# Performance work log

Hardware: AMD Instinct MI355X
Metric: run time of the kernel (lower is better)

## Reference

```python
import jax, jax.numpy as jnp
import numpy as np

B, N, C = 8, 2048, 256
E = 32768
H, C_OUT = 8, 64
NEG_SLOPE = 0.2


def setup_inputs() -> dict:
    key = jax.random.key(0)
    k1, k2, k3, k4, k5 = jax.random.split(key, 5)
    x = jax.random.normal(k1, (B, N, C), dtype=jnp.float32)
    edge_index = jax.random.randint(k2, (2, E), 0, N, dtype=jnp.int64)
    W_lin = jax.random.normal(k3, (C, H * C_OUT), dtype=jnp.float32) * 0.05
    att_src = jax.random.normal(k4, (H, C_OUT), dtype=jnp.float32) * 0.05
    att_dst = jax.random.normal(k5, (H, C_OUT), dtype=jnp.float32) * 0.05
    bias = jnp.zeros((H * C_OUT,), dtype=jnp.float32)
    return {"x": x, "edge_index": edge_index, "W_lin": W_lin,
            "att_src": att_src, "att_dst": att_dst, "bias": bias}


def _segment_softmax(logits, segment_ids, num_segments):
    # stable softmax over edges grouped by destination node
    seg_max = jax.ops.segment_max(logits, segment_ids, num_segments=num_segments)
    logits = logits - seg_max[segment_ids]
    exp = jnp.exp(logits)
    seg_sum = jax.ops.segment_sum(exp, segment_ids, num_segments=num_segments)
    return exp / (seg_sum[segment_ids] + 1e-16)


def reference(x, edge_index, W_lin, att_src, att_dst, bias):
    Bn = B * N
    # node linear projection -> [B*N, H, C_out]
    xt = (x.reshape(Bn, C) @ W_lin).reshape(Bn, H, C_OUT)

    # batch the shared edge_index: block b offset by b*N, then append self-loops
    offs = (jnp.arange(B, dtype=edge_index.dtype) * N)[None, :, None]  # [1,B,1]
    ei = (edge_index[:, None, :] + offs).reshape(2, B * E)              # [2,B*E]
    loops = jnp.arange(Bn, dtype=edge_index.dtype)
    src = jnp.concatenate([ei[0], loops])
    dst = jnp.concatenate([ei[1], loops])

    x_j = xt[src]  # [E_tot, H, C_out] source features
    x_i = xt[dst]
    alpha = jnp.einsum('ehc,hc->eh', x_j, att_src) + jnp.einsum('ehc,hc->eh', x_i, att_dst)
    alpha = jax.nn.leaky_relu(alpha, NEG_SLOPE)
    alpha = _segment_softmax(alpha, dst, Bn)  # softmax over incoming edges per node/head

    msg = x_j * alpha[:, :, None]
    out = jax.ops.segment_sum(msg, dst, num_segments=Bn)  # [B*N, H, C_out]
    out = out.reshape(B, N, H * C_OUT) + bias
    return out
```

## Files before the change

kernel.cpp:

```cpp
#include <hip/hip_runtime.h>
#include <hip/hip_bf16.h>

#define BDIM 8
#define NNODE 2048
#define CIN 256
#define NEDGE 32768
#define NHEAD 8
#define COUT 64
#define HC 512
#define BN_TOT 16384
#define NEG_SLOPE 0.2f
#define GEMM_BLKS 256
#define SCAT_BLKS 64
#define CAP 64

typedef __hip_bfloat16 bf16;
typedef __attribute__((ext_vector_type(8))) short bfrag;
typedef __attribute__((ext_vector_type(4))) float ffrag;
typedef float f32x2 __attribute__((ext_vector_type(2)));
typedef float fv4 __attribute__((ext_vector_type(4)));

static __device__ __forceinline__ short f2b(float f) {
    __hip_bfloat16 h = __float2bfloat16(f);
    return *(short*)&h;
}
static __device__ __forceinline__ unsigned pack2(float a, float b) {
    return (unsigned)(unsigned short)f2b(a) | ((unsigned)(unsigned short)f2b(b) << 16);
}
static __device__ __forceinline__ void pkfma(f32x2& a, f32x2 x, f32x2 w) {
    asm("v_pk_fma_f32 %0, %1, %2, %0" : "+v"(a) : "v"(x), "v"(w));
}
static __device__ __forceinline__ f32x2 unpack2(unsigned v) {
    f32x2 r;
    r.x = __uint_as_float(v << 16);
    r.y = __uint_as_float(v & 0xffff0000u);
    return r;
}
static __device__ __forceinline__ void async_cp16(const short* gsrc, short* ldst) {
    __builtin_amdgcn_global_load_lds(
        (const __attribute__((address_space(1))) void*)gsrc,
        (__attribute__((address_space(3))) void*)ldst, 16, 0, 0);
}

__global__ __launch_bounds__(256) void prep_kernel(const float* __restrict__ W,
                                                   short* __restrict__ WT,
                                                   int* __restrict__ cnt) {
    const int b = blockIdx.x;
    if (b < 128) {
        __shared__ float t[32][33];
        const int kt = b >> 4;
        const int nt = b & 15;
        const int tx = threadIdx.x & 31, ty = threadIdx.x >> 5;
#pragma unroll
        for (int i = 0; i < 4; ++i)
            t[ty + 8 * i][tx] = W[(kt * 32 + ty + 8 * i) * HC + nt * 32 + tx];
        __syncthreads();
#pragma unroll
        for (int i = 0; i < 4; ++i)
            WT[(nt * 32 + ty + 8 * i) * CIN + kt * 32 + tx] = f2b(t[tx][ty + 8 * i]);
    } else {
        for (int k = threadIdx.x; k < NNODE; k += 256) cnt[k] = 0;
    }
}

__global__ __launch_bounds__(512, 2) void gemm_scatter(const float* __restrict__ x,
                                                       const short* __restrict__ WT,
                                                       short* __restrict__ xtb,
                                                       const float* __restrict__ att_src,
                                                       const float* __restrict__ att_dst,
                                                       float* __restrict__ ssrc,
                                                       float* __restrict__ sdst,
                                                       const int* __restrict__ ei,
                                                       int* __restrict__ cnt,
                                                       int* __restrict__ col) {
    const int blk = blockIdx.x;
    if (blk < SCAT_BLKS) {
        const int t = blk * 512 + threadIdx.x;
        const int s = ei[t];
        const int d = ei[NEDGE + t];
        const int p = atomicAdd(&cnt[d], 1);
        if (p < CAP) col[d * CAP + p] = s;
        return;
    }

    __shared__ __align__(16) short As[64 * 256];
    __shared__ __align__(16) short Bs[2][512 * 32];

    const int gblk = blk - SCAT_BLKS;
    const int tile = (gblk & 7) * 32 + (gblk >> 3);
    const int tid  = threadIdx.x;
    const int lane = tid & 63;
    const int w    = tid >> 6;
    const int row0 = tile * 64;
    const int wm   = (w & 1) * 32;
    const int wn   = (w >> 1) * 128;
    const int fm   = lane & 15;
    const int fq   = lane >> 4;

    {
        const int r   = tid >> 3;
        const int kb0 = (tid & 7) * 8;
#pragma unroll
        for (int i = 0; i < 4; ++i) {
            const int kb = kb0 + i * 64;
            fv4 v0 = __builtin_nontemporal_load((const fv4*)&x[(row0 + r) * CIN + kb]);
            fv4 v1 = __builtin_nontemporal_load((const fv4*)&x[(row0 + r) * CIN + kb + 4]);
            bfrag o;
            o[0] = f2b(v0.x); o[1] = f2b(v0.y); o[2] = f2b(v0.z); o[3] = f2b(v0.w);
            o[4] = f2b(v1.x); o[5] = f2b(v1.y); o[6] = f2b(v1.z); o[7] = f2b(v1.w);
            *(bfrag*)&As[(((r >> 4) * 32 + (kb >> 3)) * 16 + (r & 15)) * 8] = o;
        }
    }

    {
#pragma unroll
        for (int i2 = 0; i2 < 4; ++i2) {
            const int cb16 = w * 4 + i2;
            const int c = cb16 * 16 + (lane >> 2);
            async_cp16(&WT[c * CIN + (lane & 3) * 8], &Bs[0][cb16 * 512]);
        }
    }
    __syncthreads();

    ffrag acc[8][2] = {};

    for (int k8 = 0; k8 < 8; ++k8) {
        const int buf = k8 & 1;
        if (k8 < 7) {
            const int k0n = (k8 + 1) * 32;
#pragma unroll
            for (int i2 = 0; i2 < 4; ++i2) {
                const int cb16 = w * 4 + i2;
                const int c = cb16 * 16 + (lane >> 2);
                async_cp16(&WT[c * CIN + k0n + (lane & 3) * 8], &Bs[buf ^ 1][cb16 * 512]);
            }
        }
        bfrag af[2];
#pragma unroll
        for (int mg = 0; mg < 2; ++mg)
            af[mg] = *(const bfrag*)&As[((((wm >> 4) + mg) * 32 + k8 * 4 + fq) * 16 + fm) * 8];
#pragma unroll
        for (int ng = 0; ng < 8; ++ng) {
            bfrag bfr = *(const bfrag*)&Bs[buf][((((wn >> 4) + ng) * 16 + fm) * 4 + fq) * 8];
#pragma unroll
            for (int mg = 0; mg < 2; ++mg)
                acc[ng][mg] = __builtin_amdgcn_mfma_f32_16x16x32_bf16(
                    bfr, af[mg], acc[ng][mg], 0, 0, 0);
        }
        __syncthreads();
    }

    float4 s4[8], d4[8];
#pragma unroll
    for (int ng = 0; ng < 8; ++ng) {
        const int cb = wn + ng * 16 + fq * 4;
        s4[ng] = *(const float4*)&att_src[cb];
        d4[ng] = *(const float4*)&att_dst[cb];
    }
    const int head0 = wn >> 6;
#pragma unroll
    for (int mg = 0; mg < 2; ++mg) {
        const int nd = row0 + wm + mg * 16 + fm;
        float ps0 = 0.f, pd0 = 0.f, ps1 = 0.f, pd1 = 0.f;
#pragma unroll
        for (int ng = 0; ng < 8; ++ng) {
            const int cb = wn + ng * 16 + fq * 4;
            uint2 pk;
            pk.x = pack2(acc[ng][mg][0], acc[ng][mg][1]);
            pk.y = pack2(acc[ng][mg][2], acc[ng][mg][3]);
            *(uint2*)&xtb[nd * HC + cb] = pk;
            const float dot_s = acc[ng][mg][0] * s4[ng].x + acc[ng][mg][1] * s4[ng].y +
                                acc[ng][mg][2] * s4[ng].z + acc[ng][mg][3] * s4[ng].w;
            const float dot_d = acc[ng][mg][0] * d4[ng].x + acc[ng][mg][1] * d4[ng].y +
                                acc[ng][mg][2] * d4[ng].z + acc[ng][mg][3] * d4[ng].w;
            if (ng < 4) { ps0 += dot_s; pd0 += dot_d; }
            else        { ps1 += dot_s; pd1 += dot_d; }
        }
        ps0 += __shfl_xor(ps0, 16); ps0 += __shfl_xor(ps0, 32);
        pd0 += __shfl_xor(pd0, 16); pd0 += __shfl_xor(pd0, 32);
        ps1 += __shfl_xor(ps1, 16); ps1 += __shfl_xor(ps1, 32);
        pd1 += __shfl_xor(pd1, 16); pd1 += __shfl_xor(pd1, 32);
        if (lane < 16) {
            ssrc[nd * NHEAD + head0]     = ps0;
            sdst[nd * NHEAD + head0]     = pd0;
            ssrc[nd * NHEAD + head0 + 1] = ps1;
            sdst[nd * NHEAD + head0 + 1] = pd1;
        }
    }
}

__global__ __launch_bounds__(256) void aggregate(const short* __restrict__ xtb,
                                                 const float* __restrict__ ssrc,
                                                 const float* __restrict__ sdst,
                                                 const int* __restrict__ cnt,
                                                 const int* __restrict__ col,
                                                 const float* __restrict__ bias,
                                                 float* __restrict__ out) {
    __shared__ float wlds[4][NHEAD][68];
    __shared__ int   jlds[4][64];
    const int nb   = threadIdx.x >> 6;
    const int lane = threadIdx.x & 63;
    const int blk  = blockIdx.x;
    const int bidx = blk & 7;
    const int boff = bidx * NNODE;
    const int i    = boff + (blk >> 3) * 4 + nb;
    const int n    = i & (NNODE - 1);
    const int deg  = min(cnt[n], CAP);
    const int start = n * CAP;
    const int h    = lane >> 3;
    const int sub  = lane & 7;
    float* wrow = &wlds[nb][0][0];
    int*   jrow = &jlds[nb][0];

    for (int t = lane; t < NHEAD * 68; t += 64) wrow[t] = 0.f;
    jrow[lane] = i;

    const float sdh = sdst[i * NHEAD + h];
    float selfv = ssrc[i * NHEAD + h] + sdh;
    selfv = selfv >= 0.f ? selfv : NEG_SLOPE * selfv;
    const float eself = __expf(selfv);

    float sp = 0.f;
    for (int e = sub; e < deg; e += 8) {
        int j = boff + col[start + e];
        float v = ssrc[j * NHEAD + h] + sdh;
        v = v >= 0.f ? v : NEG_SLOPE * v;
        float wv = __expf(v);
        wrow[h * 68 + e] = wv;
        if (h == 0) jrow[e] = j;
        sp += wv;
    }
    sp += __shfl_xor(sp, 4); sp += __shfl_xor(sp, 2); sp += __shfl_xor(sp, 1);
    const float inv = 1.f / (sp + eself + 1e-16f);

    const int c8 = lane * 8;
    f32x2 acc2[4] = {};

    {
        uint4 xv = *(const uint4*)&xtb[i * HC + c8];
        f32x2 ev = {eself, eself};
        pkfma(acc2[0], unpack2(xv.x), ev);
        pkfma(acc2[1], unpack2(xv.y), ev);
        pkfma(acc2[2], unpack2(xv.z), ev);
        pkfma(acc2[3], unpack2(xv.w), ev);
    }

    const int degp = (deg + 7) & ~7;
    for (int e0 = 0; e0 < degp; e0 += 8) {
        float4 wA = *(const float4*)&wrow[h * 68 + e0];
        float4 wB = *(const float4*)&wrow[h * 68 + e0 + 4];
        int4 jA = *(const int4*)&jrow[e0];
        int4 jB = *(const int4*)&jrow[e0 + 4];
        uint4 x0 = *(const uint4*)&xtb[jA.x * HC + c8];
        uint4 x1 = *(const uint4*)&xtb[jA.y * HC + c8];
        uint4 x2 = *(const uint4*)&xtb[jA.z * HC + c8];
        uint4 x3 = *(const uint4*)&xtb[jA.w * HC + c8];
        uint4 x4 = *(const uint4*)&xtb[jB.x * HC + c8];
        uint4 x5 = *(const uint4*)&xtb[jB.y * HC + c8];
        uint4 x6 = *(const uint4*)&xtb[jB.z * HC + c8];
        uint4 x7 = *(const uint4*)&xtb[jB.w * HC + c8];
        f32x2 w0 = {wA.x, wA.x}, w1 = {wA.y, wA.y}, w2 = {wA.z, wA.z}, w3 = {wA.w, wA.w};
        f32x2 w4 = {wB.x, wB.x}, w5 = {wB.y, wB.y}, w6 = {wB.z, wB.z}, w7 = {wB.w, wB.w};
#define ACC_EDGE(xv, wv)                       \
        pkfma(acc2[0], unpack2(xv.x), wv);     \
        pkfma(acc2[1], unpack2(xv.y), wv);     \
        pkfma(acc2[2], unpack2(xv.z), wv);     \
        pkfma(acc2[3], unpack2(xv.w), wv);
        ACC_EDGE(x0, w0) ACC_EDGE(x1, w1) ACC_EDGE(x2, w2) ACC_EDGE(x3, w3)
        ACC_EDGE(x4, w4) ACC_EDGE(x5, w5) ACC_EDGE(x6, w6) ACC_EDGE(x7, w7)
#undef ACC_EDGE
    }

    const float4 b0 = *(const float4*)&bias[c8];
    const float4 b1 = *(const float4*)&bias[c8 + 4];
    fv4 o0 = {acc2[0].x * inv + b0.x, acc2[0].y * inv + b0.y,
              acc2[1].x * inv + b0.z, acc2[1].y * inv + b0.w};
    fv4 o1 = {acc2[2].x * inv + b1.x, acc2[2].y * inv + b1.y,
              acc2[3].x * inv + b1.z, acc2[3].y * inv + b1.w};
    __builtin_nontemporal_store(o0, (fv4*)&out[i * HC + c8]);
    __builtin_nontemporal_store(o1, (fv4*)&out[i * HC + c8 + 4]);
}

extern "C" void kernel_launch(void* const* d_in, const int* in_sizes, int n_in,
                              void* d_out, int out_size, void* d_ws, size_t ws_size,
                              hipStream_t stream) {
    const float* x       = (const float*)d_in[0];
    const int*   ei      = (const int*)d_in[1];
    const float* W       = (const float*)d_in[2];
    const float* att_src = (const float*)d_in[3];
    const float* att_dst = (const float*)d_in[4];
    const float* bias    = (const float*)d_in[5];
    float* out = (float*)d_out;

    char* ws = (char*)d_ws;
    short* xtb  = (short*)(ws);
    float* ssrc = (float*)(ws + 16777216);
    float* sdst = (float*)(ws + 17301504);
    int*   cnt  = (int*)(ws + 17825792);
    int*   col  = (int*)(ws + 17833984);
    short* WT   = (short*)(ws + 18358272);
    prep_kernel<<<129, 256, 0, stream>>>(W, WT, cnt);
    gemm_scatter<<<GEMM_BLKS + SCAT_BLKS, 512, 0, stream>>>(x, WT, xtb, att_src, att_dst,
                                                            ssrc, sdst, ei, cnt, col);
    aggregate<<<BN_TOT / 4, 256, 0, stream>>>(xtb, ssrc, sdst, cnt, col, bias, out);
}
```

Baseline: 124.8 us.

## Give each wave one head's 64x64 tile and drop block barriers in the GEMM loop

Each wave now computes a 64-row by 64-column tile, one full head, instead of a 32x128 slice. It therefore loads only its own B columns, so the per-step __syncthreads is replaced by explicit s_waitcnt on vector and LDS counters plus sched barriers. The k-loop is fully unrolled. The attention-score reduction is also simpler, since each wave now owns exactly one head. The risks are higher register pressure from the 4x4 accumulator array and relying on hand-written waitcnt values to keep the async copies ordered correctly.

```diff
diff --git a/kernel.cpp b/kernel.cpp
--- a/kernel.cpp
+++ b/kernel.cpp
@@ -92,8 +92,6 @@
     const int lane = tid & 63;
     const int w    = tid >> 6;
     const int row0 = tile * 64;
-    const int wm   = (w & 1) * 32;
-    const int wn   = (w >> 1) * 128;
     const int fm   = lane & 15;
     const int fq   = lane >> 4;
 
@@ -122,11 +120,14 @@
     }
     __syncthreads();
 
-    ffrag acc[8][2] = {};
-
+    ffrag acc[4][4] = {};
+
+#pragma unroll
     for (int k8 = 0; k8 < 8; ++k8) {
         const int buf = k8 & 1;
         if (k8 < 7) {
+            asm volatile("s_waitcnt lgkmcnt(0)" ::: "memory");
+            __builtin_amdgcn_sched_barrier(0);
             const int k0n = (k8 + 1) * 32;
 #pragma unroll
             for (int i2 = 0; i2 < 4; ++i2) {
@@ -134,57 +135,55 @@
                 const int c = cb16 * 16 + (lane >> 2);
                 async_cp16(&WT[c * CIN + k0n + (lane & 3) * 8], &Bs[buf ^ 1][cb16 * 512]);
             }
-        }
-        bfrag af[2];
-#pragma unroll
-        for (int mg = 0; mg < 2; ++mg)
-            af[mg] = *(const bfrag*)&As[((((wm >> 4) + mg) * 32 + k8 * 4 + fq) * 16 + fm) * 8];
-#pragma unroll
-        for (int ng = 0; ng < 8; ++ng) {
-            bfrag bfr = *(const bfrag*)&Bs[buf][((((wn >> 4) + ng) * 16 + fm) * 4 + fq) * 8];
-#pragma unroll
-            for (int mg = 0; mg < 2; ++mg)
-                acc[ng][mg] = __builtin_amdgcn_mfma_f32_16x16x32_bf16(
-                    bfr, af[mg], acc[ng][mg], 0, 0, 0);
-        }
-        __syncthreads();
-    }
-
-    float4 s4[8], d4[8];
-#pragma unroll
-    for (int ng = 0; ng < 8; ++ng) {
-        const int cb = wn + ng * 16 + fq * 4;
+            asm volatile("s_waitcnt vmcnt(4)" ::: "memory");
+        } else {
+            asm volatile("s_waitcnt vmcnt(0)" ::: "memory");
+        }
+        __builtin_amdgcn_sched_barrier(0);
+
+        bfrag af[4], bfv[4];
+#pragma unroll
+        for (int mg = 0; mg < 4; ++mg)
+            af[mg] = *(const bfrag*)&As[((mg * 32 + k8 * 4 + fq) * 16 + fm) * 8];
+#pragma unroll
+        for (int ng = 0; ng < 4; ++ng)
+            bfv[ng] = *(const bfrag*)&Bs[buf][(((w * 4 + ng) * 16 + fm) * 4 + fq) * 8];
+#pragma unroll
+        for (int ng = 0; ng < 4; ++ng)
+#pragma unroll
+            for (int mg = 0; mg < 4; ++mg)
+                acc[mg][ng] = __builtin_amdgcn_mfma_f32_16x16x32_bf16(
+                    bfv[ng], af[mg], acc[mg][ng], 0, 0, 0);
+    }
+
+    float4 s4[4], d4[4];
+#pragma unroll
+    for (int ng = 0; ng < 4; ++ng) {
+        const int cb = w * 64 + ng * 16 + fq * 4;
         s4[ng] = *(const float4*)&att_src[cb];
         d4[ng] = *(const float4*)&att_dst[cb];
     }
-    const int head0 = wn >> 6;
-#pragma unroll
-    for (int mg = 0; mg < 2; ++mg) {
-        const int nd = row0 + wm + mg * 16 + fm;
-        float ps0 = 0.f, pd0 = 0.f, ps1 = 0.f, pd1 = 0.f;
-#pragma unroll
-        for (int ng = 0; ng < 8; ++ng) {
-            const int cb = wn + ng * 16 + fq * 4;
+#pragma unroll
+    for (int mg = 0; mg < 4; ++mg) {
+        const int nd = row0 + mg * 16 + fm;
+        float ps = 0.f, pd = 0.f;
+#pragma unroll
+        for (int ng = 0; ng < 4; ++ng) {
+            const int cb = w * 64 + ng * 16 + fq * 4;
             uint2 pk;
-            pk.x = pack2(acc[ng][mg][0], acc[ng][mg][1]);
-            pk.y = pack2(acc[ng][mg][2], acc[ng][mg][3]);
+            pk.x = pack2(acc[mg][ng][0], acc[mg][ng][1]);
+            pk.y = pack2(acc[mg][ng][2], acc[mg][ng][3]);
             *(uint2*)&xtb[nd * HC + cb] = pk;
-            const float dot_s = acc[ng][mg][0] * s4[ng].x + acc[ng][mg][1] * s4[ng].y +
-                                acc[ng][mg][2] * s4[ng].z + acc[ng][mg][3] * s4[ng].w;
-            const float dot_d = acc[ng][mg][0] * d4[ng].x + acc[ng][mg][1] * d4[ng].y +
-                                acc[ng][mg][2] * d4[ng].z + acc[ng][mg][3] * d4[ng].w;
-            if (ng < 4) { ps0 += dot_s; pd0 += dot_d; }
-            else        { ps1 += dot_s; pd1 += dot_d; }
-        }
-        ps0 += __shfl_xor(ps0, 16); ps0 += __shfl_xor(ps0, 32);
-        pd0 += __shfl_xor(pd0, 16); pd0 += __shfl_xor(pd0, 32);
-        ps1 += __shfl_xor(ps1, 16); ps1 += __shfl_xor(ps1, 32);
-        pd1 += __shfl_xor(pd1, 16); pd1 += __shfl_xor(pd1, 32);
+            ps += acc[mg][ng][0] * s4[ng].x + acc[mg][ng][1] * s4[ng].y +
+                  acc[mg][ng][2] * s4[ng].z + acc[mg][ng][3] * s4[ng].w;
+            pd += acc[mg][ng][0] * d4[ng].x + acc[mg][ng][1] * d4[ng].y +
+                  acc[mg][ng][2] * d4[ng].z + acc[mg][ng][3] * d4[ng].w;
+        }
+        ps += __shfl_xor(ps, 16); ps += __shfl_xor(ps, 32);
+        pd += __shfl_xor(pd, 16); pd += __shfl_xor(pd, 32);
         if (lane < 16) {
-            ssrc[nd * NHEAD + head0]     = ps0;
-            sdst[nd * NHEAD + head0]     = pd0;
-            ssrc[nd * NHEAD + head0 + 1] = ps1;
-            sdst[nd * NHEAD + head0 + 1] = pd1;
+            ssrc[nd * NHEAD + w] = ps;
+            sdst[nd * NHEAD + w] = pd;
         }
     }
 }
```

New measurement: 123.8 us. No clear change (-0.8%).
